# Performance work log

Hardware: AMD Instinct MI355X
Metric: run time of the kernel (lower is better)

The kernel has to match this reference:

```python
import jax, jax.numpy as jnp
import numpy as np

H, DH = 12, 64            # num heads, head dim (hidden=768)
ATTN_WINDOW = 512         # Longformer attention_window
W = ATTN_WINDOW // 2      # one-sided window (attend W tokens each side + self)


def setup_inputs() -> dict:
    key = jax.random.key(0)
    ks = jax.random.split(key, 4)
    B, S, D = 2, 4096, 768
    sc = 0.02
    return {
        "hidden_states": jax.random.normal(ks[0], (B, S, D), jnp.float32),
        "attention_mask": jnp.zeros((B, S), jnp.float32),  # 0 = normal local attention
        "Wq": jax.random.normal(ks[1], (D, D), jnp.float32) * sc,
        "bq": jnp.zeros((D,), jnp.float32),
        "Wk": jax.random.normal(ks[2], (D, D), jnp.float32) * sc,
        "bk": jnp.zeros((D,), jnp.float32),
        "Wv": jax.random.normal(ks[3], (D, D), jnp.float32) * sc,
        "bv": jnp.zeros((D,), jnp.float32),
    }


def _windows(x):
    # x: [B, H, nb+2, w, D] overlapping 3-block windows -> [B, H, nb, 3w, D]
    return jnp.concatenate([x[:, :, :-2], x[:, :, 1:-1], x[:, :, 2:]], axis=3)


def reference(hidden_states, attention_mask, Wq, bq, Wk, bk, Wv, bv):
    B, S, D = hidden_states.shape
    w = W
    nb = S // w  # number of query blocks

    # QKV projections; Longformer scales q by 1/sqrt(head_dim)
    q = (hidden_states @ Wq + bq) / jnp.sqrt(jnp.asarray(DH, hidden_states.dtype))
    k = hidden_states @ Wk + bk
    v = hidden_states @ Wv + bv

    def split_heads(x):  # [B,S,D] -> [B,H,S,DH]
        return x.reshape(B, S, H, DH).transpose(0, 2, 1, 3)

    q, k, v = split_heads(q), split_heads(k), split_heads(v)

    qb = q.reshape(B, H, nb, w, DH)
    kp = jnp.pad(k, ((0, 0), (0, 0), (w, w), (0, 0))).reshape(B, H, nb + 2, w, DH)
    vp = jnp.pad(v, ((0, 0), (0, 0), (w, w), (0, 0))).reshape(B, H, nb + 2, w, DH)
    kw, vw = _windows(kp), _windows(vp)  # [B,H,nb,3w,DH]

    # banded scores: each query block attends its 3w key window
    scores = jnp.einsum('bhnqd,bhnkd->bhnqk', qb, kw)  # [B,H,nb,w,3w]

    # sliding-window diagonal mask: |i - j| <= w and key index in [0, S)
    q_idx = (jnp.arange(nb) * w)[:, None] + jnp.arange(w)[None, :]          # [nb,w]
    k_idx = (jnp.arange(nb) * w - w)[:, None] + jnp.arange(3 * w)[None, :]  # [nb,3w]
    rel = k_idx[:, None, :] - q_idx[:, :, None]                              # [nb,w,3w]
    in_win = (jnp.abs(rel) <= w) & (k_idx[:, None, :] >= 0) & (k_idx[:, None, :] < S)

    # key padding mask (attention_mask < 0 => masked token)
    masked = attention_mask < 0  # [B,S]
    kmp = jnp.pad(masked, ((0, 0), (w, w))).reshape(B, nb + 2, w)
    kmw = jnp.concatenate([kmp[:, :-2], kmp[:, 1:-1], kmp[:, 2:]], axis=2)  # [B,nb,3w]

    allowed = in_win[None, None] & ~kmw[:, None, :, None, :]  # [B,H,nb,w,3w]
    scores = jnp.where(allowed, scores, jnp.asarray(-1e9, scores.dtype))

    probs = jax.nn.softmax(scores, axis=-1)
    # zero out attention rows of masked (padding) queries, as Longformer does
    probs = jnp.where(masked.reshape(B, 1, nb, w, 1), jnp.zeros((), probs.dtype), probs)

    out = jnp.einsum('bhnqk,bhnkd->bhnqd', probs, vw)  # [B,H,nb,w,DH]
    out = out.reshape(B, H, S, DH).transpose(0, 2, 1, 3).reshape(B, S, H * DH)
    return out
```

## Files before the change

kernel.cpp:

```cpp
#include <hip/hip_runtime.h>
#include <hip/hip_bf16.h>

#define BATCH 2
#define SEQ   4096
#define DM    768
#define NHEAD 12
#define HDIM  64
#define WIN   256

typedef unsigned short u16;
typedef unsigned int u32;
typedef __attribute__((ext_vector_type(8))) short bf16x8;
typedef __attribute__((ext_vector_type(4))) float f32x4;
typedef __attribute__((ext_vector_type(8))) unsigned short u16x8;
typedef __attribute__((ext_vector_type(4))) unsigned short u16x4;
typedef __attribute__((ext_vector_type(2))) unsigned int u32x2;

__device__ __forceinline__ u16 f2bf(float x) {
    unsigned u = __builtin_bit_cast(unsigned, x);
    return (u16)((u + 0x7FFFu + ((u >> 16) & 1u)) >> 16);
}

#define GLL16(g, l) __builtin_amdgcn_global_load_lds( \
    (const __attribute__((address_space(1))) u32*)(g), \
    (__attribute__((address_space(3))) u32*)(l), 16, 0, 0)

__global__ __launch_bounds__(256) void prep(
    const float* __restrict__ in, u16* __restrict__ Abf,
    const float* __restrict__ Wq, const float* __restrict__ Wk,
    const float* __restrict__ Wv, u16* __restrict__ Wt)
{
    __shared__ float tile[32][33];
    const int bid = blockIdx.x;
    if (bid < 3072) {
        size_t i = ((size_t)bid * 256 + threadIdx.x) * 8;
        float4 a = *(const float4*)(in + i);
        float4 b = *(const float4*)(in + i + 4);
        u16x8 r;
        r[0] = f2bf(a.x); r[1] = f2bf(a.y); r[2] = f2bf(a.z); r[3] = f2bf(a.w);
        r[4] = f2bf(b.x); r[5] = f2bf(b.y); r[6] = f2bf(b.z); r[7] = f2bf(b.w);
        *(u16x8*)(Abf + i) = r;
    } else {
        const int wb = bid - 3072;
        const int mat = wb / 576;
        const int rem = wb - mat * 576;
        const int k0 = (rem / 24) * 32, n0 = (rem % 24) * 32;
        const float* W = (mat == 0) ? Wq : (mat == 1) ? Wk : Wv;
        const int tx = threadIdx.x & 31, ty = threadIdx.x >> 5;
        #pragma unroll
        for (int i = 0; i < 32; i += 8)
            tile[ty + i][tx] = W[(size_t)(k0 + ty + i) * DM + n0 + tx];
        __syncthreads();
        #pragma unroll
        for (int i = 0; i < 32; i += 8)
            Wt[(size_t)mat * DM * DM + (size_t)(n0 + ty + i) * DM + k0 + tx] = f2bf(tile[tx][ty + i]);
    }
}

__global__ __launch_bounds__(256) void qkv_mfma(
    const u16* __restrict__ Abf, const u16* __restrict__ Wt,
    const float* __restrict__ bq, const float* __restrict__ bk, const float* __restrict__ bv,
    u16* __restrict__ qo, u16* __restrict__ ko, u16* __restrict__ vT)
{
    __shared__ u16 As[2][128][32];
    __shared__ u16 Bs[2][128][32];

    const int t  = threadIdx.x;
    const int wv = t >> 6, ln = t & 63, lg = ln >> 4, lm = ln & 15;
    const int wr = wv >> 1, wc = wv & 1;

    const int id  = blockIdx.x + 18 * blockIdx.y;
    const int nid = (id & 7) * 144 + (id >> 3);
    const int bx  = nid % 18, by = nid / 18;

    const int rowStart = by * 128;
    const int nG = bx * 128;
    const int mat = nG / DM;
    const int nColBase = nG - mat * DM;
    const float* bias = (mat == 0) ? bq : (mat == 1) ? bk : bv;
    const u16* Wm = Wt + (size_t)mat * DM * DM;

    f32x4 acc[4][4];
    #pragma unroll
    for (int i = 0; i < 4; i++)
        #pragma unroll
        for (int j = 0; j < 4; j++) acc[i][j] = (f32x4){0.f, 0.f, 0.f, 0.f};

    const int srow0 = wv * 16 + (ln >> 2);
    const int scol  = (ln & 3) * 8;
    u16* ldsA0 = &As[0][0][0] + wv * 512 + ln * 8;
    u16* ldsB0 = &Bs[0][0][0] + wv * 512 + ln * 8;
    const u16* gA = Abf + (size_t)(rowStart + srow0) * DM + scol;
    const u16* gB = Wm  + (size_t)(nColBase + srow0) * DM + scol;

    #define STAGE(buf, k0) do { \
        u16* la_ = ldsA0 + (buf) * 4096; \
        u16* lb_ = ldsB0 + (buf) * 4096; \
        GLL16(gA + (k0), la_); \
        GLL16(gA + (size_t)64 * DM + (k0), la_ + 2048); \
        GLL16(gB + (k0), lb_); \
        GLL16(gB + (size_t)64 * DM + (k0), lb_ + 2048); \
    } while (0)

    STAGE(0, 0);
    __syncthreads();
    int cur = 0;

    for (int it = 0; it < 24; ++it) {
        const int k0 = it * 32;
        if (it < 23) STAGE(cur ^ 1, k0 + 32);
        bf16x8 af[4], bfr[4];
        #pragma unroll
        for (int mi = 0; mi < 4; mi++) af[mi]  = *(const bf16x8*)&As[cur][wr * 64 + mi * 16 + lm][lg * 8];
        #pragma unroll
        for (int ni = 0; ni < 4; ni++) bfr[ni] = *(const bf16x8*)&Bs[cur][wc * 64 + ni * 16 + lm][lg * 8];
        __builtin_amdgcn_s_setprio(1);
        #pragma unroll
        for (int mi = 0; mi < 4; mi++)
            #pragma unroll
            for (int ni = 0; ni < 4; ni++)
                acc[mi][ni] = __builtin_amdgcn_mfma_f32_16x16x32_bf16(af[mi], bfr[ni], acc[mi][ni], 0, 0, 0);
        __builtin_amdgcn_s_setprio(0);
        __syncthreads();
        cur ^= 1;
    }

    const int bb = rowStart >> 12;
    const int s0base = (rowStart & 4095) + wr * 64;
    const int col0 = nColBase + wc * 64;
    #pragma unroll
    for (int ni = 0; ni < 4; ni++) {
        const int col = col0 + ni * 16 + lm;
        const int h = col >> 6, d = col & 63;
        const float bsv = bias[col];
        #pragma unroll
        for (int mi = 0; mi < 4; mi++) {
            const int srow = s0base + mi * 16 + lg * 4;
            if (mat == 2) {
                u16x4 pk;
                #pragma unroll
                for (int r = 0; r < 4; r++) pk[r] = f2bf(acc[mi][ni][r] + bsv);
                *(u16x4*)(vT + ((size_t)((bb * NHEAD + h) * HDIM + d)) * SEQ + srow) = pk;
            } else {
                u16* dst = (mat == 0) ? qo : ko;
                const float scl = (mat == 0) ? 0.18033688011112042f : 1.f;
                #pragma unroll
                for (int r = 0; r < 4; r++)
                    dst[((size_t)(bb * NHEAD + h) * SEQ + srow + r) * HDIM + d] =
                        f2bf((acc[mi][ni][r] + bsv) * scl);
            }
        }
    }
}

__global__ __launch_bounds__(256, 4) void attn_mfma(
    const u16* __restrict__ Q, const u16* __restrict__ K,
    const u16* __restrict__ vT, const float* __restrict__ amask,
    float* __restrict__ out)
{
    __shared__ u16 Ks[2][64][64];
    __shared__ u16 Vs[2][64][64];
    __shared__ u16 Pl[4][16][64];

    const int t  = threadIdx.x;
    const int wv = t >> 6, ln = t & 63, lg = ln >> 4, lm = ln & 15;
    const int lm7 = lm & 7;

    const int id  = blockIdx.x + 64 * (blockIdx.y + 12 * blockIdx.z);
    const int nid = (id & 7) * 192 + (id >> 3);
    const int qtile = nid & 63;
    const int hb = nid >> 6;
    const int h = hb % NHEAD, b = hb / NHEAD;

    const int qb0 = qtile * 64;
    const size_t bh = (size_t)(b * NHEAD + h);
    const size_t bS = (size_t)b * SEQ;

    const int qrow = qb0 + wv * 16 + lm;
    const bf16x8 qa0 = *(const bf16x8*)(Q + (bh * SEQ + qrow) * HDIM + lg * 8);
    const bf16x8 qa1 = *(const bf16x8*)(Q + (bh * SEQ + qrow) * HDIM + 32 + lg * 8);

    f32x4 po[4];
    #pragma unroll
    for (int i = 0; i < 4; i++) po[i] = (f32x4){0.f, 0.f, 0.f, 0.f};
    float mrun = -1e9f, lrun = 0.f;

    const int tlo = (4 - qtile) > 0 ? (4 - qtile) : 0;
    const int thi_raw = (SEQ + 192 - qb0) >> 6;
    const int thi = thi_raw < 8 ? thi_raw : 8;

    u16x8 kreg[2], vreg[2];

    auto load_regs = [&](int tt) {
        const int jt0 = qb0 - WIN + tt * 64;
        #pragma unroll
        for (int i = 0; i < 2; i++) {
            int cid = t + i * 256;
            int row = cid >> 3, c = cid & 7;
            kreg[i] = *(const u16x8*)(K  + (bh * SEQ + jt0 + row) * HDIM + c * 8);
            vreg[i] = *(const u16x8*)(vT + (bh * HDIM + row) * SEQ + jt0 + c * 8);
        }
    };
    auto write_lds = [&](int buf) {
        #pragma unroll
        for (int i = 0; i < 2; i++) {
            int cid = t + i * 256;
            int row = cid >> 3, c = cid & 7;
            *(u16x8*)&Ks[buf][row][(c ^ (row & 7)) * 8] = kreg[i];
            *(u16x8*)&Vs[buf][row][(c ^ (row & 7)) * 8] = vreg[i];
        }
    };

    load_regs(tlo);
    write_lds(0);
    __syncthreads();
    int cur = 0;

    for (int tt = tlo; tt <= thi; ++tt) {
        const int jt0 = qb0 - WIN + tt * 64;
        const float kmv = amask[bS + jt0 + ln];
        if (tt < thi) load_regs(tt + 1);

        f32x4 sv[4];
        #pragma unroll
        for (int jf = 0; jf < 4; jf++) sv[jf] = (f32x4){0.f, 0.f, 0.f, 0.f};
        __builtin_amdgcn_s_setprio(1);
        #pragma unroll
        for (int jf = 0; jf < 4; jf++) {
            const u16* kr = &Ks[cur][jf * 16 + lm][0];
            bf16x8 kb0 = *(const bf16x8*)(kr + ((lg ^ lm7) << 3));
            bf16x8 kb1 = *(const bf16x8*)(kr + (((4 + lg) ^ lm7) << 3));
            sv[jf] = __builtin_amdgcn_mfma_f32_16x16x32_bf16(kb0, qa0, sv[jf], 0, 0, 0);
            sv[jf] = __builtin_amdgcn_mfma_f32_16x16x32_bf16(kb1, qa1, sv[jf], 0, 0, 0);
        }
        __builtin_amdgcn_s_setprio(0);

        const bool anym = (__ballot(kmv < 0.f) != 0ULL);
        const bool fastp = (tt >= 1) && (tt <= 7) && !anym;
        if (!fastp) {
            #pragma unroll
            for (int jf = 0; jf < 4; jf++)
                #pragma unroll
                for (int r = 0; r < 4; r++) {
                    const int j = jt0 + jf * 16 + lg * 4 + r;
                    const float km = __shfl(kmv, jf * 16 + lg * 4 + r);
                    const int rel = j - qrow;
                    const bool ok = (rel <= WIN) && (rel >= -WIN) && (km >= 0.f);
                    sv[jf][r] = ok ? sv[jf][r] : -1e9f;
                }
        }

        f32x4 mv = sv[0];
        #pragma unroll
        for (int jf = 1; jf < 4; jf++) {
            mv[0] = fmaxf(mv[0], sv[jf][0]); mv[1] = fmaxf(mv[1], sv[jf][1]);
            mv[2] = fmaxf(mv[2], sv[jf][2]); mv[3] = fmaxf(mv[3], sv[jf][3]);
        }
        float mx = fmaxf(fmaxf(mv[0], mv[1]), fmaxf(mv[2], mv[3]));
        mx = fmaxf(mx, __shfl_xor(mx, 16));
        mx = fmaxf(mx, __shfl_xor(mx, 32));
        const float mnew = fmaxf(mrun, mx);
        const float f = exp2f(mrun - mnew);
        mrun = mnew;

        float p[4][4];
        if (fastp) {
            #pragma unroll
            for (int jf = 0; jf < 4; jf++)
                #pragma unroll
                for (int r = 0; r < 4; r++) p[jf][r] = exp2f(sv[jf][r] - mnew);
        } else {
            #pragma unroll
            for (int jf = 0; jf < 4; jf++)
                #pragma unroll
                for (int r = 0; r < 4; r++)
                    p[jf][r] = sv[jf][r] > -1e8f ? exp2f(sv[jf][r] - mnew) : 0.f;
        }

        float ps = 0.f;
        #pragma unroll
        for (int jf = 0; jf < 4; jf++)
            ps += (p[jf][0] + p[jf][1]) + (p[jf][2] + p[jf][3]);
        ps += __shfl_xor(ps, 16);
        ps += __shfl_xor(ps, 32);
        lrun = lrun * f + ps;

        u32* prow = (u32*)&Pl[wv][lm][0];
        #pragma unroll
        for (int jf = 0; jf < 4; jf++) {
            u32 lo, hi;
            asm("v_cvt_pk_bf16_f32 %0, %1, %2" : "=v"(lo) : "v"(p[jf][0]), "v"(p[jf][1]));
            asm("v_cvt_pk_bf16_f32 %0, %1, %2" : "=v"(hi) : "v"(p[jf][2]), "v"(p[jf][3]));
            const int c = 2 * jf + (lg >> 1);
            u32x2 val; val[0] = lo; val[1] = hi;
            *(u32x2*)(prow + ((c ^ lm7) << 2) + ((lg & 1) << 1)) = val;
        }
        asm volatile("" ::: "memory");

        po[0] *= f; po[1] *= f; po[2] *= f; po[3] *= f;

        const u16* pw = &Pl[wv][lm][0];
        const bf16x8 pa0 = *(const bf16x8*)(pw + ((lg ^ lm7) << 3));
        const bf16x8 pa1 = *(const bf16x8*)(pw + (((4 + lg) ^ lm7) << 3));
        __builtin_amdgcn_s_setprio(1);
        #pragma unroll
        for (int df = 0; df < 4; df++) {
            const u16* vr = &Vs[cur][df * 16 + lm][0];
            bf16x8 va0 = *(const bf16x8*)(vr + ((lg ^ lm7) << 3));
            bf16x8 va1 = *(const bf16x8*)(vr + (((4 + lg) ^ lm7) << 3));
            po[df] = __builtin_amdgcn_mfma_f32_16x16x32_bf16(va0, pa0, po[df], 0, 0, 0);
            po[df] = __builtin_amdgcn_mfma_f32_16x16x32_bf16(va1, pa1, po[df], 0, 0, 0);
        }
        __builtin_amdgcn_s_setprio(0);

        if (tt < thi) write_lds(cur ^ 1);
        __syncthreads();
        cur ^= 1;
    }

    const float qm = amask[bS + qrow];
    const float inv = (lrun > 0.f && qm >= 0.f) ? 1.f / lrun : 0.f;
    float* op = out + (bS + qrow) * DM + h * HDIM;
    #pragma unroll
    for (int df = 0; df < 4; df++) {
        f32x4 o = po[df] * inv;
        *(f32x4*)(op + df * 16 + lg * 4) = o;
    }
}

extern "C" void kernel_launch(void* const* d_in, const int* in_sizes, int n_in,
                              void* d_out, int out_size, void* d_ws, size_t ws_size,
                              hipStream_t stream) {
    const float* hs    = (const float*)d_in[0];
    const float* amask = (const float*)d_in[1];
    const float* Wq    = (const float*)d_in[2];
    const float* bq    = (const float*)d_in[3];
    const float* Wk    = (const float*)d_in[4];
    const float* bk    = (const float*)d_in[5];
    const float* Wv    = (const float*)d_in[6];
    const float* bv    = (const float*)d_in[7];

    const size_t nA   = (size_t)BATCH * SEQ * DM;
    const size_t nW   = (size_t)3 * DM * DM;
    const size_t nQKV = (size_t)BATCH * NHEAD * SEQ * HDIM;

    u16* Abf = (u16*)d_ws;
    u16* Wt  = Abf + nA;
    u16* qb  = Wt + nW;
    u16* kb  = qb + nQKV;
    u16* vT  = kb + nQKV;

    prep<<<4800, 256, 0, stream>>>(hs, Abf, Wq, Wk, Wv, Wt);
    qkv_mfma<<<dim3(3 * DM / 128, BATCH * SEQ / 128), 256, 0, stream>>>(
        Abf, Wt, bq, bk, bv, qb, kb, vT);
    attn_mfma<<<dim3(SEQ / 64, NHEAD, BATCH), 256, 0, stream>>>(
        qb, kb, vT, amask, (float*)d_out);
}
```

Baseline: 102.2 us.

## Triple-buffer QKV GEMM LDS staging with swizzled layout and vmcnt waits

Replaces the QKV projection GEMM's double-buffered LDS staging with a three-stage ring. Prefetches now run two K-steps ahead, and each step waits with a partial vmcnt plus a single barrier instead of a full syncthreads. The global-to-LDS addressing is also remapped with an XOR swizzle, so the 16-byte fragment reads spread across LDS banks. The aim is to hide global load latency and cut bank conflicts, at the cost of more LDS and hand-managed wait counts that must match the number of outstanding loads.

```diff
diff --git a/kernel.cpp b/kernel.cpp
--- a/kernel.cpp
+++ b/kernel.cpp
@@ -62,8 +62,7 @@
     const float* __restrict__ bq, const float* __restrict__ bk, const float* __restrict__ bv,
     u16* __restrict__ qo, u16* __restrict__ ko, u16* __restrict__ vT)
 {
-    __shared__ u16 As[2][128][32];
-    __shared__ u16 Bs[2][128][32];
+    __shared__ u16 lds[3 * 8192];
 
     const int t  = threadIdx.x;
     const int wv = t >> 6, ln = t & 63, lg = ln >> 4, lm = ln & 15;
@@ -86,34 +85,40 @@
         #pragma unroll
         for (int j = 0; j < 4; j++) acc[i][j] = (f32x4){0.f, 0.f, 0.f, 0.f};
 
-    const int srow0 = wv * 16 + (ln >> 2);
-    const int scol  = (ln & 3) * 8;
-    u16* ldsA0 = &As[0][0][0] + wv * 512 + ln * 8;
-    u16* ldsB0 = &Bs[0][0][0] + wv * 512 + ln * 8;
-    const u16* gA = Abf + (size_t)(rowStart + srow0) * DM + scol;
-    const u16* gB = Wm  + (size_t)(nColBase + srow0) * DM + scol;
-
-    #define STAGE(buf, k0) do { \
-        u16* la_ = ldsA0 + (buf) * 4096; \
-        u16* lb_ = ldsB0 + (buf) * 4096; \
-        GLL16(gA + (k0), la_); \
-        GLL16(gA + (size_t)64 * DM + (k0), la_ + 2048); \
-        GLL16(gB + (k0), lb_); \
-        GLL16(gB + (size_t)64 * DM + (k0), lb_ + 2048); \
-    } while (0)
-
-    STAGE(0, 0);
-    __syncthreads();
-    int cur = 0;
-
-    for (int it = 0; it < 24; ++it) {
-        const int k0 = it * 32;
-        if (it < 23) STAGE(cur ^ 1, k0 + 32);
+    int r0, c0, r1, c1;
+    {
+        int byte0 = t * 16;
+        int rp = byte0 >> 7, s = (byte0 >> 4) & 7, cf = s ^ (rp & 7);
+        r0 = 2 * rp + (cf >> 2); c0 = cf & 3;
+        int byte1 = 4096 + t * 16;
+        rp = byte1 >> 7; s = (byte1 >> 4) & 7; cf = s ^ (rp & 7);
+        r1 = 2 * rp + (cf >> 2); c1 = cf & 3;
+    }
+    const u16* gA0 = Abf + (size_t)(rowStart + r0) * DM + c0 * 8;
+    const u16* gA1 = Abf + (size_t)(rowStart + r1) * DM + c1 * 8;
+    const u16* gB0 = Wm  + (size_t)(nColBase + r0) * DM + c0 * 8;
+    const u16* gB1 = Wm  + (size_t)(nColBase + r1) * DM + c1 * 8;
+
+    auto STAGE = [&](int buf, int k0) {
+        u16* base = lds + buf * 8192 + t * 8;
+        GLL16(gA0 + k0, base);
+        GLL16(gA1 + k0, base + 2048);
+        GLL16(gB0 + k0, base + 4096);
+        GLL16(gB1 + k0, base + 6144);
+    };
+
+    auto SWO = [&](int row, int lgc) -> int {
+        return ((row >> 1) << 6) + (((((row & 1) << 2) + lgc) ^ ((row >> 1) & 7)) << 3);
+    };
+
+    auto COMPUTE = [&](int buf) {
+        const u16* Ab = lds + buf * 8192;
+        const u16* Bb = Ab + 4096;
         bf16x8 af[4], bfr[4];
         #pragma unroll
-        for (int mi = 0; mi < 4; mi++) af[mi]  = *(const bf16x8*)&As[cur][wr * 64 + mi * 16 + lm][lg * 8];
-        #pragma unroll
-        for (int ni = 0; ni < 4; ni++) bfr[ni] = *(const bf16x8*)&Bs[cur][wc * 64 + ni * 16 + lm][lg * 8];
+        for (int mi = 0; mi < 4; mi++) af[mi]  = *(const bf16x8*)(Ab + SWO(wr * 64 + mi * 16 + lm, lg));
+        #pragma unroll
+        for (int ni = 0; ni < 4; ni++) bfr[ni] = *(const bf16x8*)(Bb + SWO(wc * 64 + ni * 16 + lm, lg));
         __builtin_amdgcn_s_setprio(1);
         #pragma unroll
         for (int mi = 0; mi < 4; mi++)
@@ -121,9 +126,24 @@
             for (int ni = 0; ni < 4; ni++)
                 acc[mi][ni] = __builtin_amdgcn_mfma_f32_16x16x32_bf16(af[mi], bfr[ni], acc[mi][ni], 0, 0, 0);
         __builtin_amdgcn_s_setprio(0);
-        __syncthreads();
-        cur ^= 1;
-    }
+    };
+
+    STAGE(0, 0);
+    STAGE(1, 32);
+    int cur = 0;
+    for (int it = 0; it < 23; ++it) {
+        asm volatile("s_waitcnt vmcnt(4)" ::: "memory");
+        __builtin_amdgcn_s_barrier();
+        if (it < 22) {
+            int nb = cur + 2; if (nb >= 3) nb -= 3;
+            STAGE(nb, (it + 2) * 32);
+        }
+        COMPUTE(cur);
+        cur = (cur == 2) ? 0 : cur + 1;
+    }
+    asm volatile("s_waitcnt vmcnt(0)" ::: "memory");
+    __builtin_amdgcn_s_barrier();
+    COMPUTE(cur);
 
     const int bb = rowStart >> 12;
     const int s0base = (rowStart & 4095) + wr * 64;
```

Result: faster. 94.31 us (-7.7%).
